# Kernel tuning notes

Measured on AMD Instinct MI355X. Metric: run time of the kernel, lower is better.

Reference implementation:

```python
import jax, jax.numpy as jnp
import numpy as np

B, S, D = 2, 2048, 1024   # batch, seq, d_model
E, F, K = 8, 2048, 2      # num_experts, ffn_hidden_size, top_k


def setup_inputs() -> dict:
    key = jax.random.key(0)
    ks = jax.random.split(key, 5)
    scale = 0.02
    hidden_states = jax.random.normal(ks[0], (B, S, D), dtype=jnp.float32)
    router_kernel = jax.random.normal(ks[1], (D, E), dtype=jnp.float32) * scale
    # expert params, already reshaped to (E, F, D) as in DbrxExpertGLU.expert_shape
    w1 = jax.random.normal(ks[2], (E, F, D), dtype=jnp.float32) * scale
    v1 = jax.random.normal(ks[3], (E, F, D), dtype=jnp.float32) * scale
    w2 = jax.random.normal(ks[4], (E, F, D), dtype=jnp.float32) * scale
    return {"hidden_states": hidden_states, "router_kernel": router_kernel,
            "w1": w1, "v1": v1, "w2": w2}


def reference(hidden_states, router_kernel, w1, v1, w2):
    # ---- Router ----
    logits = jnp.einsum('bsd,de->bse', hidden_states.astype(jnp.float32), router_kernel)
    weights = jax.nn.softmax(logits, axis=-1)                # [B,S,E]
    top_weights, top_experts = jax.lax.top_k(weights, K)     # [B,S,K]
    # moe_normalize_expert_weights = 1 -> L1 normalization
    top_weights = top_weights / jnp.sum(jnp.abs(top_weights), axis=-1, keepdims=True)
    weights = weights.astype(hidden_states.dtype)
    top_weights = top_weights.astype(hidden_states.dtype)
    # ---- Experts: every expert's GLU over all tokens, masked accumulation ----
    out = jnp.zeros_like(hidden_states)
    for e in range(E):  # small fixed expert count; matches original loop
        x1 = jnp.einsum('bsd,fd->bsf', hidden_states, w1[e])   # [B,S,F]
        x2 = jnp.einsum('bsd,fd->bsf', hidden_states, v1[e])
        h = jax.nn.silu(x1) * x2
        y_e = jnp.einsum('bsf,fd->bsd', h, w2[e])               # [B,S,D]
        gate = jnp.sum((top_experts == e) * top_weights, axis=-1)  # [B,S]
        out = out + gate[:, :, None] * y_e
    return out, weights
```

## Files before the change

### kernel.cpp

```cpp
#include <hip/hip_runtime.h>
#include <stdint.h>
#include <math.h>

#define NB 2
#define NS 2048
#define ND 1024
#define NE 8
#define NF 2048
#define NTOK (NB*NS)
#define EFD ((size_t)NE*NF*ND)
#define NROWS (2*NTOK)

typedef short bf16x8 __attribute__((ext_vector_type(8)));
typedef float f32x4 __attribute__((ext_vector_type(4)));

__device__ __forceinline__ unsigned short f2bf(float f) {
  unsigned u = __float_as_uint(f);
  unsigned r = (u + 0x7FFFu + ((u >> 16) & 1u)) >> 16;
  return (unsigned short)r;
}
__device__ __forceinline__ float bf2f(unsigned short s) {
  return __uint_as_float(((unsigned)s) << 16);
}

__device__ __forceinline__ void async16(unsigned short* lds, const unsigned short* g) {
  __builtin_amdgcn_global_load_lds(
      (const __attribute__((address_space(1))) unsigned int*)g,
      (__attribute__((address_space(3))) unsigned int*)lds, 16, 0, 0);
}

#define VMCNT(n) asm volatile("s_waitcnt vmcnt(" #n ")" ::: "memory")
#define LGKM0    asm volatile("s_waitcnt lgkmcnt(0)" ::: "memory")
#define SBAR     __builtin_amdgcn_s_barrier()
#define SCHED0   __builtin_amdgcn_sched_barrier(0)

__global__ void cvt_bf16(const float* __restrict__ src,
                         unsigned short* __restrict__ dst, int n4) {
  int i = blockIdx.x * blockDim.x + threadIdx.x;
  int stride = gridDim.x * blockDim.x;
  for (; i < n4; i += stride) {
    float4 v = ((const float4*)src)[i];
    ushort4 o;
    o.x = f2bf(v.x); o.y = f2bf(v.y); o.z = f2bf(v.z); o.w = f2bf(v.w);
    ((ushort4*)dst)[i] = o;
  }
}

__global__ void transpose_w2(const float* __restrict__ w2,
                             unsigned short* __restrict__ w2t) {
  __shared__ float tile[32][33];
  int e = blockIdx.z;
  int d0 = blockIdx.x * 32, f0 = blockIdx.y * 32;
  int tx = threadIdx.x, ty = threadIdx.y;
  const float* src = w2 + (size_t)e * NF * ND;
  unsigned short* dst = w2t + (size_t)e * ND * NF;
#pragma unroll
  for (int i = ty; i < 32; i += 8)
    tile[i][tx] = src[(size_t)(f0 + i) * ND + d0 + tx];
  __syncthreads();
#pragma unroll
  for (int i = ty; i < 32; i += 8)
    dst[(size_t)(d0 + i) * NF + f0 + tx] = f2bf(tile[tx][i]);
}

__global__ void router_kernel(const float* __restrict__ hs,
                              const float* __restrict__ rk,
                              float* __restrict__ wout,
                              float* __restrict__ tw,
                              int* __restrict__ choice,
                              unsigned short* __restrict__ hsb) {
  int lane = threadIdx.x;
  int tt = lane & 15, part = lane >> 4;
  int t = blockIdx.x * 16 + tt;
  const float4* hrow = (const float4*)(hs + (size_t)t * ND) + part * 64;
  ushort4* hb4 = (ushort4*)(hsb + (size_t)t * ND) + part * 64;
  const float4* rk4 = (const float4*)rk + part * 512;
  float acc[NE];
#pragma unroll
  for (int e = 0; e < NE; ++e) acc[e] = 0.f;
#pragma unroll 4
  for (int i = 0; i < 64; ++i) {
    float4 x = hrow[i];
    ushort4 o;
    o.x = f2bf(x.x); o.y = f2bf(x.y); o.z = f2bf(x.z); o.w = f2bf(x.w);
    hb4[i] = o;
    float xs[4] = {x.x, x.y, x.z, x.w};
#pragma unroll
    for (int j = 0; j < 4; ++j) {
      float4 r0 = rk4[i * 8 + j * 2];
      float4 r1 = rk4[i * 8 + j * 2 + 1];
      acc[0] += xs[j] * r0.x; acc[1] += xs[j] * r0.y;
      acc[2] += xs[j] * r0.z; acc[3] += xs[j] * r0.w;
      acc[4] += xs[j] * r1.x; acc[5] += xs[j] * r1.y;
      acc[6] += xs[j] * r1.z; acc[7] += xs[j] * r1.w;
    }
  }
#pragma unroll
  for (int e = 0; e < NE; ++e) {
    acc[e] += __shfl_xor(acc[e], 16, 64);
    acc[e] += __shfl_xor(acc[e], 32, 64);
  }
  if (part == 0) {
    float mx = acc[0]; int i0 = 0;
#pragma unroll
    for (int e = 1; e < NE; ++e) if (acc[e] > mx) { mx = acc[e]; i0 = e; }
    float m2 = -3.4e38f; int i1 = 0;
#pragma unroll
    for (int e = 0; e < NE; ++e) if (e != i0 && acc[e] > m2) { m2 = acc[e]; i1 = e; }
    float p[NE]; float den = 0.f;
#pragma unroll
    for (int e = 0; e < NE; ++e) { p[e] = expf(acc[e] - mx); den += p[e]; }
    float inv = 1.f / den;
#pragma unroll
    for (int e = 0; e < NE; ++e) { p[e] *= inv; wout[t * NE + e] = p[e]; }
    float w0 = p[i0], w1 = p[i1];
    float s = 1.f / (w0 + w1);
    tw[t * 2 + 0] = w0 * s;
    tw[t * 2 + 1] = w1 * s;
    choice[t] = i0 | (i1 << 4);
  }
}

__global__ void build_lists(const int* __restrict__ choice,
                            int* __restrict__ counts,
                            int* __restrict__ off,
                            int* __restrict__ list,
                            int* __restrict__ posn) {
  __shared__ int lcnt[NE];
  int tid = threadIdx.x;
  if (tid < NE) lcnt[tid] = 0;
  __syncthreads();
  int4 c4 = ((const int4*)choice)[tid];
  int cs[4] = {c4.x, c4.y, c4.z, c4.w};
#pragma unroll
  for (int j = 0; j < 4; ++j) {
    int t = tid * 4 + j;
    int e0 = cs[j] & 15, e1 = (cs[j] >> 4) & 15;
    int p0 = atomicAdd(&lcnt[e0], 1);
    list[e0 * NTOK + p0] = t << 1;
    int p1 = atomicAdd(&lcnt[e1], 1);
    list[e1 * NTOK + p1] = (t << 1) | 1;
    posn[t] = p0 | (p1 << 16);
  }
  __syncthreads();
  if (tid == 0) {
    int s = 0;
#pragma unroll
    for (int e = 0; e < NE; ++e) { counts[e] = lcnt[e]; off[e] = s; s += lcnt[e]; }
    off[NE] = s;
  }
}

__global__ __launch_bounds__(256, 2) void gemm_fused(
    const int* __restrict__ counts, const int* __restrict__ off,
    const int* __restrict__ list,
    const unsigned short* __restrict__ A,
    const unsigned short* __restrict__ B1,
    const unsigned short* __restrict__ B2,
    unsigned short* __restrict__ H) {
  int bid = blockIdx.x;
  int e = bid >> 9;
  int rem = bid & 511;
  int mt = rem >> 4, nt = rem & 15;
  int cnt = counts[e];
  if (mt * 128 >= cnt) return;
  int off_e = off[e];

  __shared__ unsigned short lds[2][12288];

  int tid = threadIdx.x;
  int wid = tid >> 6, lane = tid & 63;
  int wr = wid >> 1, wc = wid & 1;
  int l15 = lane & 15, l4 = lane >> 4;
  const int* mylist = list + e * NTOK;

  int trow = tid >> 2;
  int co = ((tid & 3) ^ ((tid >> 3) & 3)) * 8;
  const unsigned short* aS0;
  const unsigned short* aS1;
  {
    int r0 = mt * 128 + trow;
    int r1 = r0 + 64;
    if (r0 >= cnt) r0 = cnt - 1;
    if (r1 >= cnt) r1 = cnt - 1;
    int e0 = mylist[r0], e1 = mylist[r1];
    aS0 = A + (size_t)(e0 >> 1) * ND + co;
    aS1 = A + (size_t)(e1 >> 1) * ND + co;
  }
  const unsigned short* b1S0 = B1 + (size_t)e * NF * ND + (size_t)(nt * 128 + trow) * ND + co;
  const unsigned short* b1S1 = b1S0 + (size_t)64 * ND;
  const unsigned short* b2S0 = B2 + (size_t)e * NF * ND + (size_t)(nt * 128 + trow) * ND + co;
  const unsigned short* b2S1 = b2S0 + (size_t)64 * ND;

  int rowA[4], rowB[4];
#pragma unroll
  for (int mi = 0; mi < 4; ++mi) {
    int r = wr * 64 + mi * 16 + l15;
    rowA[mi] = r * 64 + ((l4 ^ ((r >> 1) & 3)) << 4);
  }
#pragma unroll
  for (int ni = 0; ni < 4; ++ni) {
    int r = wc * 64 + ni * 16 + l15;
    rowB[ni] = r * 64 + ((l4 ^ ((r >> 1) & 3)) << 4);
  }

  f32x4 acc1[4][4], acc2[4][4];
#pragma unroll
  for (int mi = 0; mi < 4; ++mi)
#pragma unroll
    for (int ni = 0; ni < 4; ++ni) {
      f32x4 z = {0.f, 0.f, 0.f, 0.f};
      acc1[mi][ni] = z; acc2[mi][ni] = z;
    }

  auto STAGE = [&](int c, int kt) {
    int ko = kt * 32;
    unsigned short* base = &lds[c][0] + tid * 8;
    async16(base,         aS0 + ko);
    async16(base + 2048,  aS1 + ko);
    async16(base + 4096,  b1S0 + ko);
    async16(base + 6144,  b1S1 + ko);
    async16(base + 8192,  b2S0 + ko);
    async16(base + 10240, b2S1 + ko);
  };

  const int kT = ND / 32;
  STAGE(0, 0); STAGE(1, 1);

  for (int kt = 0; kt < kT; ++kt) {
    int cur = kt & 1;
    if (kt + 1 < kT) { VMCNT(6); }
    else             { VMCNT(0); }
    SCHED0;
    SBAR;

    const char* la = (const char*)&lds[cur][0];
    const char* lb1 = la + 8192;
    const char* lb2 = la + 16384;
    bf16x8 a[4], b1[4], b2[4];
#pragma unroll
    for (int mi = 0; mi < 4; ++mi)
      a[mi] = *(const bf16x8*)(la + rowA[mi]);
#pragma unroll
    for (int ni = 0; ni < 4; ++ni) {
      b1[ni] = *(const bf16x8*)(lb1 + rowB[ni]);
      b2[ni] = *(const bf16x8*)(lb2 + rowB[ni]);
    }
    LGKM0;
    SCHED0;
    SBAR;
    if (kt + 2 < kT) STAGE(cur, kt + 2);

    __builtin_amdgcn_s_setprio(1);
#pragma unroll
    for (int mi = 0; mi < 4; ++mi)
#pragma unroll
      for (int ni = 0; ni < 4; ++ni) {
        acc1[mi][ni] = __builtin_amdgcn_mfma_f32_16x16x32_bf16(
            a[mi], b1[ni], acc1[mi][ni], 0, 0, 0);
        acc2[mi][ni] = __builtin_amdgcn_mfma_f32_16x16x32_bf16(
            a[mi], b2[ni], acc2[mi][ni], 0, 0, 0);
      }
    __builtin_amdgcn_s_setprio(0);
  }

  int rowbase = mt * 128 + wr * 64;
  int colbase = nt * 128 + wc * 64;
#pragma unroll
  for (int mi = 0; mi < 4; ++mi) {
#pragma unroll
    for (int j = 0; j < 4; ++j) {
      int r = rowbase + mi * 16 + l4 * 4 + j;
      if (r >= cnt) continue;
      size_t row = (size_t)(off_e + r);
#pragma unroll
      for (int ni = 0; ni < 4; ++ni) {
        int c = colbase + ni * 16 + l15;
        float x1 = acc1[mi][ni][j];
        float x2 = acc2[mi][ni][j];
        float h = (x1 / (1.f + expf(-x1))) * x2;
        H[row * NF + c] = f2bf(h);
      }
    }
  }
}

__global__ __launch_bounds__(256, 2) void gemm_p3(
    const int* __restrict__ counts, const int* __restrict__ off,
    const unsigned short* __restrict__ Ah,
    const unsigned short* __restrict__ Bw,
    unsigned short* __restrict__ Y) {
  int bid = blockIdx.x;
  int e = bid >> 8;
  int rem = bid & 255;
  int mt = rem >> 3;
  int code = rem & 7;
  int nt = code >> 1, kh = code & 1;
  int cnt = counts[e];
  if (mt * 128 >= cnt) return;
  int off_e = off[e];

  __shared__ unsigned short lds[2][12288];

  int tid = threadIdx.x;
  int wid = tid >> 6, lane = tid & 63;
  int wr = wid >> 1, wc = wid & 1;
  int l15 = lane & 15, l4 = lane >> 4;

  int trow = tid >> 2;
  int co = ((tid & 3) ^ ((tid >> 3) & 3)) * 8;
  const unsigned short* aS[2];
#pragma unroll
  for (int g = 0; g < 2; ++g) {
    int r = mt * 128 + g * 64 + trow;
    if (r >= cnt) r = cnt - 1;
    aS[g] = Ah + (size_t)(off_e + r) * NF + kh * 1024 + co;
  }
  const unsigned short* bS[4];
#pragma unroll
  for (int g = 0; g < 4; ++g) {
    int d = nt * 256 + g * 64 + trow;
    bS[g] = Bw + (size_t)e * ND * NF + (size_t)d * NF + kh * 1024 + co;
  }

  int rowA[4], rowB[8];
#pragma unroll
  for (int mi = 0; mi < 4; ++mi) {
    int r = wr * 64 + mi * 16 + l15;
    rowA[mi] = r * 64 + ((l4 ^ ((r >> 1) & 3)) << 4);
  }
#pragma unroll
  for (int ni = 0; ni < 8; ++ni) {
    int r = wc * 128 + ni * 16 + l15;
    rowB[ni] = 8192 + r * 64 + ((l4 ^ ((r >> 1) & 3)) << 4);
  }

  f32x4 acc[4][8];
#pragma unroll
  for (int mi = 0; mi < 4; ++mi)
#pragma unroll
    for (int ni = 0; ni < 8; ++ni) {
      f32x4 z = {0.f, 0.f, 0.f, 0.f};
      acc[mi][ni] = z;
    }

  auto STAGE = [&](int c, int kt) {
    int ko = kt * 32;
    unsigned short* base = &lds[c][0] + tid * 8;
    async16(base,         aS[0] + ko);
    async16(base + 2048,  aS[1] + ko);
    async16(base + 4096,  bS[0] + ko);
    async16(base + 6144,  bS[1] + ko);
    async16(base + 8192,  bS[2] + ko);
    async16(base + 10240, bS[3] + ko);
  };

  const int kT = 32;
  STAGE(0, 0); STAGE(1, 1);

  for (int kt = 0; kt < kT; ++kt) {
    int cur = kt & 1;
    if (kt + 1 < kT) { VMCNT(6); }
    else             { VMCNT(0); }
    SCHED0;
    SBAR;

    const char* buf = (const char*)&lds[cur][0];
    bf16x8 a[4], b[8];
#pragma unroll
    for (int mi = 0; mi < 4; ++mi)
      a[mi] = *(const bf16x8*)(buf + rowA[mi]);
#pragma unroll
    for (int ni = 0; ni < 8; ++ni)
      b[ni] = *(const bf16x8*)(buf + rowB[ni]);
    LGKM0;
    SCHED0;
    SBAR;
    if (kt + 2 < kT) STAGE(cur, kt + 2);

    __builtin_amdgcn_s_setprio(1);
#pragma unroll
    for (int mi = 0; mi < 4; ++mi)
#pragma unroll
      for (int ni = 0; ni < 8; ++ni)
        acc[mi][ni] = __builtin_amdgcn_mfma_f32_16x16x32_bf16(
            a[mi], b[ni], acc[mi][ni], 0, 0, 0);
    __builtin_amdgcn_s_setprio(0);
  }

  unsigned short* Yp = Y + (size_t)kh * NROWS * ND;
#pragma unroll
  for (int mi = 0; mi < 4; ++mi)
#pragma unroll
    for (int j = 0; j < 4; ++j) {
      int r = mt * 128 + wr * 64 + mi * 16 + l4 * 4 + j;
      if (r >= cnt) continue;
      size_t row = (size_t)(off_e + r);
#pragma unroll
      for (int ni = 0; ni < 8; ++ni) {
        int d = nt * 256 + wc * 128 + ni * 16 + l15;
        Yp[row * ND + d] = f2bf(acc[mi][ni][j]);
      }
    }
}

__global__ void combine_kernel(const unsigned short* __restrict__ yc,
                               const float* __restrict__ tw,
                               const int* __restrict__ choice,
                               const int* __restrict__ posn,
                               const int* __restrict__ off,
                               float* __restrict__ out) {
  int t = blockIdx.x;
  int tid = threadIdx.x;
  int ch = choice[t];
  int pp = posn[t];
  int e0 = ch & 15, e1 = (ch >> 4) & 15;
  size_t r0 = (size_t)(off[e0] + (pp & 0xffff));
  size_t r1 = (size_t)(off[e1] + (pp >> 16));
  float w0 = tw[t * 2], w1 = tw[t * 2 + 1];
  const size_t P = (size_t)NROWS * ND;
  ushort4 a0 = ((const ushort4*)(yc + r0 * ND))[tid];
  ushort4 b0 = ((const ushort4*)(yc + P + r0 * ND))[tid];
  ushort4 a1 = ((const ushort4*)(yc + r1 * ND))[tid];
  ushort4 b1 = ((const ushort4*)(yc + P + r1 * ND))[tid];
  float4 o;
  o.x = w0 * (bf2f(a0.x) + bf2f(b0.x)) + w1 * (bf2f(a1.x) + bf2f(b1.x));
  o.y = w0 * (bf2f(a0.y) + bf2f(b0.y)) + w1 * (bf2f(a1.y) + bf2f(b1.y));
  o.z = w0 * (bf2f(a0.z) + bf2f(b0.z)) + w1 * (bf2f(a1.z) + bf2f(b1.z));
  o.w = w0 * (bf2f(a0.w) + bf2f(b0.w)) + w1 * (bf2f(a1.w) + bf2f(b1.w));
  ((float4*)(out + (size_t)t * ND))[tid] = o;
}


extern "C" void kernel_launch(void* const* d_in, const int* in_sizes, int n_in,
                              void* d_out, int out_size, void* d_ws, size_t ws_size,
                              hipStream_t stream) {
  const float* hs = (const float*)d_in[0];
  const float* rk = (const float*)d_in[1];
  const float* w1 = (const float*)d_in[2];
  const float* v1 = (const float*)d_in[3];
  const float* w2 = (const float*)d_in[4];
  float* out = (float*)d_out;
  float* wout = out + (size_t)NTOK * ND;

  char* ws = (char*)d_ws;
  int* counts = (int*)(ws + 0);
  int* off = (int*)(ws + 64);
  int* choice = (int*)(ws + 128);
  int* posn = (int*)(ws + 16512);
  float* tw = (float*)(ws + 32896);
  int* list = (int*)(ws + 65664);
  unsigned short* hsb = (unsigned short*)(ws + 196736);
  unsigned short* w1b = (unsigned short*)(ws + 8585344);
  unsigned short* v1b = (unsigned short*)(ws + 42139776);
  unsigned short* w2t = (unsigned short*)(ws + 75694208);
  unsigned short* hcomp = (unsigned short*)(ws + 109248640);
  unsigned short* ycomp = (unsigned short*)(ws + 142803072);

  router_kernel<<<256, 64, 0, stream>>>(hs, rk, wout, tw, choice, hsb);
  build_lists<<<1, 1024, 0, stream>>>(choice, counts, off, list, posn);

  cvt_bf16<<<4096, 256, 0, stream>>>(w1, w1b, (int)(EFD / 4));
  cvt_bf16<<<4096, 256, 0, stream>>>(v1, v1b, (int)(EFD / 4));
  transpose_w2<<<dim3(ND / 32, NF / 32, NE), dim3(32, 8), 0, stream>>>(w2, w2t);

  gemm_fused<<<4096, 256, 0, stream>>>(counts, off, list, hsb, w1b, v1b, hcomp);

  gemm_p3<<<2048, 256, 0, stream>>>(counts, off, hcomp, w2t, ycomp);

  combine_kernel<<<NTOK, 256, 0, stream>>>(ycomp, tw, choice, posn, off, out);
}
```

Measured before the change: 271.4 us.

## Unify expert GEMMs into 256x256-tile 8-wave kernel with phased LDS pipeline

Replaces the two 128-row GEMM kernels with one templated 512-thread kernel that uses 256x256 output tiles, a 64-wide K step split into two sub-steps, and a phase-interleaved schedule. Each phase issues its async loads before its MFMAs, overlapping copies with compute. In the fused W1/V1 pass the B tile stacks the W1 and V1 rows, and the GLU is applied by exchanging the V1 accumulators through LDS. The aim is more operand reuse per byte loaded and fewer blocks. The cost is about 132KB of LDS per block, more register pressure, and more wasted work on partially filled 256-row expert tiles.

```diff
diff --git a/kernel.cpp b/kernel.cpp
--- a/kernel.cpp
+++ b/kernel.cpp
@@ -151,257 +151,206 @@
   }
 }
 
-__global__ __launch_bounds__(256, 2) void gemm_fused(
+template <int FUSED>
+__global__ __launch_bounds__(512, 2) void gemm8(
     const int* __restrict__ counts, const int* __restrict__ off,
     const int* __restrict__ list,
     const unsigned short* __restrict__ A,
     const unsigned short* __restrict__ B1,
     const unsigned short* __restrict__ B2,
-    unsigned short* __restrict__ H) {
+    unsigned short* __restrict__ H,
+    unsigned short* __restrict__ Y) {
   int bid = blockIdx.x;
-  int e = bid >> 9;
-  int rem = bid & 511;
-  int mt = rem >> 4, nt = rem & 15;
+  int e, mt, nt, kh = 0;
+  if (FUSED) { e = bid >> 7; int r = bid & 127; mt = r >> 4; nt = r & 15; }
+  else       { e = bid >> 6; int r = bid & 63;  mt = r >> 3; int c = r & 7; nt = c >> 1; kh = c & 1; }
   int cnt = counts[e];
-  if (mt * 128 >= cnt) return;
+  if (mt * 256 >= cnt) return;
   int off_e = off[e];
 
-  __shared__ unsigned short lds[2][12288];
+  __shared__ char smem[135168];
 
   int tid = threadIdx.x;
   int wid = tid >> 6, lane = tid & 63;
-  int wr = wid >> 1, wc = wid & 1;
+  int wm = wid >> 2, wn = wid & 3;
   int l15 = lane & 15, l4 = lane >> 4;
   const int* mylist = list + e * NTOK;
 
-  int trow = tid >> 2;
-  int co = ((tid & 3) ^ ((tid >> 3) & 3)) * 8;
-  const unsigned short* aS0;
-  const unsigned short* aS1;
+  const unsigned short* aS0; const unsigned short* aS1;
+  const unsigned short* bS0; const unsigned short* bS1;
   {
-    int r0 = mt * 128 + trow;
-    int r1 = r0 + 64;
-    if (r0 >= cnt) r0 = cnt - 1;
-    if (r1 >= cnt) r1 = cnt - 1;
-    int e0 = mylist[r0], e1 = mylist[r1];
-    aS0 = A + (size_t)(e0 >> 1) * ND + co;
-    aS1 = A + (size_t)(e1 >> 1) * ND + co;
-  }
-  const unsigned short* b1S0 = B1 + (size_t)e * NF * ND + (size_t)(nt * 128 + trow) * ND + co;
-  const unsigned short* b1S1 = b1S0 + (size_t)64 * ND;
-  const unsigned short* b2S0 = B2 + (size_t)e * NF * ND + (size_t)(nt * 128 + trow) * ND + co;
-  const unsigned short* b2S1 = b2S0 + (size_t)64 * ND;
-
-  int rowA[4], rowB[4];
-#pragma unroll
-  for (int mi = 0; mi < 4; ++mi) {
-    int r = wr * 64 + mi * 16 + l15;
-    rowA[mi] = r * 64 + ((l4 ^ ((r >> 1) & 3)) << 4);
+#pragma unroll
+    for (int i = 0; i < 2; ++i) {
+      int slot = tid + i * 512;
+      int row = slot >> 2;
+      int co = ((slot & 3) ^ (row & 3)) * 8;
+      const unsigned short* ap;
+      const unsigned short* bp;
+      int r = mt * 256 + row;
+      if (r >= cnt) r = cnt - 1;
+      if (FUSED) {
+        int entry = mylist[r];
+        ap = A + (size_t)(entry >> 1) * ND + co;
+        bp = (row < 128)
+           ? B1 + (size_t)e * NF * ND + (size_t)(nt * 128 + row) * ND + co
+           : B2 + (size_t)e * NF * ND + (size_t)(nt * 128 + row - 128) * ND + co;
+      } else {
+        ap = A + (size_t)(off_e + r) * NF + kh * 1024 + co;
+        bp = B1 + (size_t)e * ND * NF + (size_t)(nt * 256 + row) * NF + kh * 1024 + co;
+      }
+      if (i == 0) { aS0 = ap; bS0 = bp; } else { aS1 = ap; bS1 = bp; }
+    }
+  }
+
+  int offA[8], offB[4];
+#pragma unroll
+  for (int mi = 0; mi < 8; ++mi) {
+    int row = wm * 128 + mi * 16 + l15;
+    offA[mi] = row * 64 + ((l4 ^ (row & 3)) << 4);
   }
 #pragma unroll
   for (int ni = 0; ni < 4; ++ni) {
-    int r = wc * 64 + ni * 16 + l15;
-    rowB[ni] = r * 64 + ((l4 ^ ((r >> 1) & 3)) << 4);
-  }
-
-  f32x4 acc1[4][4], acc2[4][4];
-#pragma unroll
-  for (int mi = 0; mi < 4; ++mi)
+    int row = wn * 64 + ni * 16 + l15;
+    offB[ni] = row * 64 + ((l4 ^ (row & 3)) << 4);
+  }
+
+  f32x4 acc[8][4];
+#pragma unroll
+  for (int mi = 0; mi < 8; ++mi)
 #pragma unroll
     for (int ni = 0; ni < 4; ++ni) {
       f32x4 z = {0.f, 0.f, 0.f, 0.f};
-      acc1[mi][ni] = z; acc2[mi][ni] = z;
-    }
-
-  auto STAGE = [&](int c, int kt) {
-    int ko = kt * 32;
-    unsigned short* base = &lds[c][0] + tid * 8;
-    async16(base,         aS0 + ko);
-    async16(base + 2048,  aS1 + ko);
-    async16(base + 4096,  b1S0 + ko);
-    async16(base + 6144,  b1S1 + ko);
-    async16(base + 8192,  b2S0 + ko);
-    async16(base + 10240, b2S1 + ko);
+      acc[mi][ni] = z;
+    }
+
+  auto STAGE_A = [&](int buf, int ks, int tile) {
+    if (tile < 16) {
+      int ko = tile * 64 + ks * 32;
+      unsigned short* base = (unsigned short*)(smem + buf * 65536 + ks * 16384) + tid * 8;
+      async16(base, aS0 + ko);
+      async16(base + 4096, aS1 + ko);
+    }
   };
-
-  const int kT = ND / 32;
-  STAGE(0, 0); STAGE(1, 1);
-
-  for (int kt = 0; kt < kT; ++kt) {
-    int cur = kt & 1;
-    if (kt + 1 < kT) { VMCNT(6); }
-    else             { VMCNT(0); }
-    SCHED0;
-    SBAR;
-
-    const char* la = (const char*)&lds[cur][0];
-    const char* lb1 = la + 8192;
-    const char* lb2 = la + 16384;
-    bf16x8 a[4], b1[4], b2[4];
-#pragma unroll
-    for (int mi = 0; mi < 4; ++mi)
-      a[mi] = *(const bf16x8*)(la + rowA[mi]);
-#pragma unroll
-    for (int ni = 0; ni < 4; ++ni) {
-      b1[ni] = *(const bf16x8*)(lb1 + rowB[ni]);
-      b2[ni] = *(const bf16x8*)(lb2 + rowB[ni]);
-    }
-    LGKM0;
-    SCHED0;
-    SBAR;
-    if (kt + 2 < kT) STAGE(cur, kt + 2);
-
-    __builtin_amdgcn_s_setprio(1);
-#pragma unroll
-    for (int mi = 0; mi < 4; ++mi)
-#pragma unroll
-      for (int ni = 0; ni < 4; ++ni) {
-        acc1[mi][ni] = __builtin_amdgcn_mfma_f32_16x16x32_bf16(
-            a[mi], b1[ni], acc1[mi][ni], 0, 0, 0);
-        acc2[mi][ni] = __builtin_amdgcn_mfma_f32_16x16x32_bf16(
-            a[mi], b2[ni], acc2[mi][ni], 0, 0, 0);
+  auto STAGE_B = [&](int buf, int ks, int tile) {
+    if (tile < 16) {
+      int ko = tile * 64 + ks * 32;
+      unsigned short* base = (unsigned short*)(smem + buf * 65536 + 32768 + ks * 16384) + tid * 8;
+      async16(base, bS0 + ko);
+      async16(base + 4096, bS1 + ko);
+    }
+  };
+
+  STAGE_A(0, 0, 0); STAGE_B(0, 0, 0);
+  STAGE_A(0, 1, 0); STAGE_B(0, 1, 0);
+  STAGE_A(1, 0, 1); STAGE_B(1, 0, 1);
+  VMCNT(8);
+  SCHED0;
+  SBAR;
+
+  bf16x8 bq0, bq1, bq2, bq3;
+
+#define PH(Q, BUF, MIB, KS, STG, VMT) \
+  { \
+    const char* ab = smem + (BUF) * 65536 + (KS) * 16384; \
+    const char* bb = ab + 32768; \
+    bf16x8 a0 = *(const bf16x8*)(ab + offA[(MIB) + 0]); \
+    bf16x8 a1 = *(const bf16x8*)(ab + offA[(MIB) + 1]); \
+    bf16x8 a2 = *(const bf16x8*)(ab + offA[(MIB) + 2]); \
+    bf16x8 a3 = *(const bf16x8*)(ab + offA[(MIB) + 3]); \
+    if ((Q) % 2 == 0) { \
+      bq0 = *(const bf16x8*)(bb + offB[0]); \
+      bq1 = *(const bf16x8*)(bb + offB[1]); \
+      bq2 = *(const bf16x8*)(bb + offB[2]); \
+      bq3 = *(const bf16x8*)(bb + offB[3]); \
+    } \
+    STG; \
+    SBAR; \
+    LGKM0; SCHED0; \
+    __builtin_amdgcn_s_setprio(1); \
+    acc[(MIB)+0][0] = __builtin_amdgcn_mfma_f32_16x16x32_bf16(a0, bq0, acc[(MIB)+0][0], 0, 0, 0); \
+    acc[(MIB)+0][1] = __builtin_amdgcn_mfma_f32_16x16x32_bf16(a0, bq1, acc[(MIB)+0][1], 0, 0, 0); \
+    acc[(MIB)+0][2] = __builtin_amdgcn_mfma_f32_16x16x32_bf16(a0, bq2, acc[(MIB)+0][2], 0, 0, 0); \
+    acc[(MIB)+0][3] = __builtin_amdgcn_mfma_f32_16x16x32_bf16(a0, bq3, acc[(MIB)+0][3], 0, 0, 0); \
+    acc[(MIB)+1][0] = __builtin_amdgcn_mfma_f32_16x16x32_bf16(a1, bq0, acc[(MIB)+1][0], 0, 0, 0); \
+    acc[(MIB)+1][1] = __builtin_amdgcn_mfma_f32_16x16x32_bf16(a1, bq1, acc[(MIB)+1][1], 0, 0, 0); \
+    acc[(MIB)+1][2] = __builtin_amdgcn_mfma_f32_16x16x32_bf16(a1, bq2, acc[(MIB)+1][2], 0, 0, 0); \
+    acc[(MIB)+1][3] = __builtin_amdgcn_mfma_f32_16x16x32_bf16(a1, bq3, acc[(MIB)+1][3], 0, 0, 0); \
+    acc[(MIB)+2][0] = __builtin_amdgcn_mfma_f32_16x16x32_bf16(a2, bq0, acc[(MIB)+2][0], 0, 0, 0); \
+    acc[(MIB)+2][1] = __builtin_amdgcn_mfma_f32_16x16x32_bf16(a2, bq1, acc[(MIB)+2][1], 0, 0, 0); \
+    acc[(MIB)+2][2] = __builtin_amdgcn_mfma_f32_16x16x32_bf16(a2, bq2, acc[(MIB)+2][2], 0, 0, 0); \
+    acc[(MIB)+2][3] = __builtin_amdgcn_mfma_f32_16x16x32_bf16(a2, bq3, acc[(MIB)+2][3], 0, 0, 0); \
+    acc[(MIB)+3][0] = __builtin_amdgcn_mfma_f32_16x16x32_bf16(a3, bq0, acc[(MIB)+3][0], 0, 0, 0); \
+    acc[(MIB)+3][1] = __builtin_amdgcn_mfma_f32_16x16x32_bf16(a3, bq1, acc[(MIB)+3][1], 0, 0, 0); \
+    acc[(MIB)+3][2] = __builtin_amdgcn_mfma_f32_16x16x32_bf16(a3, bq2, acc[(MIB)+3][2], 0, 0, 0); \
+    acc[(MIB)+3][3] = __builtin_amdgcn_mfma_f32_16x16x32_bf16(a3, bq3, acc[(MIB)+3][3], 0, 0, 0); \
+    __builtin_amdgcn_s_setprio(0); \
+    VMT; \
+    SBAR; \
+  }
+
+  for (int j = 0; j < 8; ++j) {
+    int t1 = 2 * j + 1, t2 = 2 * j + 2, t3 = 2 * j + 3;
+    bool last = (j == 7);
+    PH(0, 0, 0, 0, STAGE_A(1, 1, t1), {});
+    PH(1, 0, 4, 0, STAGE_B(1, 1, t1), { VMCNT(8); SCHED0; });
+    PH(2, 0, 0, 1, STAGE_A(0, 0, t2), {});
+    PH(3, 0, 4, 1, STAGE_B(0, 0, t2), { if (last) { VMCNT(4); } else { VMCNT(8); } SCHED0; });
+    PH(4, 1, 0, 0, STAGE_A(0, 1, t2), {});
+    PH(5, 1, 4, 0, STAGE_B(0, 1, t2), { if (last) { VMCNT(0); } else { VMCNT(8); } SCHED0; });
+    PH(6, 1, 0, 1, STAGE_A(1, 0, t3), {});
+    PH(7, 1, 4, 1, STAGE_B(1, 0, t3), { if (!last) { VMCNT(8); SCHED0; } });
+  }
+#undef PH
+
+  if (FUSED) {
+    float* xl = (float*)smem;
+    if (wn >= 2) {
+#pragma unroll
+      for (int mi = 0; mi < 8; ++mi)
+#pragma unroll
+        for (int jj = 0; jj < 4; ++jj) {
+          int row = wm * 128 + mi * 16 + l4 * 4 + jj;
+#pragma unroll
+          for (int ni = 0; ni < 4; ++ni)
+            xl[row * 132 + (wn - 2) * 64 + ni * 16 + l15] = acc[mi][ni][jj];
+        }
+    }
+    __syncthreads();
+    if (wn < 2) {
+#pragma unroll
+      for (int mi = 0; mi < 8; ++mi)
+#pragma unroll
+        for (int jj = 0; jj < 4; ++jj) {
+          int row = wm * 128 + mi * 16 + l4 * 4 + jj;
+          int r = mt * 256 + row;
+          if (r >= cnt) continue;
+          size_t hrow = (size_t)(off_e + r);
+#pragma unroll
+          for (int ni = 0; ni < 4; ++ni) {
+            int col = wn * 64 + ni * 16 + l15;
+            float x1 = acc[mi][ni][jj];
+            float x2 = xl[row * 132 + col];
+            float h = (x1 / (1.f + expf(-x1))) * x2;
+            H[hrow * NF + nt * 128 + col] = f2bf(h);
+          }
+        }
+    }
+  } else {
+    unsigned short* Yp = Y + (size_t)kh * NROWS * ND;
+#pragma unroll
+    for (int mi = 0; mi < 8; ++mi)
+#pragma unroll
+      for (int jj = 0; jj < 4; ++jj) {
+        int r = mt * 256 + wm * 128 + mi * 16 + l4 * 4 + jj;
+        if (r >= cnt) continue;
+        size_t row = (size_t)(off_e + r);
+#pragma unroll
+        for (int ni = 0; ni < 4; ++ni) {
+          int d = nt * 256 + wn * 64 + ni * 16 + l15;
+          Yp[row * ND + d] = f2bf(acc[mi][ni][jj]);
+        }
       }
-    __builtin_amdgcn_s_setprio(0);
-  }
-
-  int rowbase = mt * 128 + wr * 64;
-  int colbase = nt * 128 + wc * 64;
-#pragma unroll
-  for (int mi = 0; mi < 4; ++mi) {
-#pragma unroll
-    for (int j = 0; j < 4; ++j) {
-      int r = rowbase + mi * 16 + l4 * 4 + j;
-      if (r >= cnt) continue;
-      size_t row = (size_t)(off_e + r);
-#pragma unroll
-      for (int ni = 0; ni < 4; ++ni) {
-        int c = colbase + ni * 16 + l15;
-        float x1 = acc1[mi][ni][j];
-        float x2 = acc2[mi][ni][j];
-        float h = (x1 / (1.f + expf(-x1))) * x2;
-        H[row * NF + c] = f2bf(h);
-      }
-    }
-  }
-}
-
-__global__ __launch_bounds__(256, 2) void gemm_p3(
-    const int* __restrict__ counts, const int* __restrict__ off,
-    const unsigned short* __restrict__ Ah,
-    const unsigned short* __restrict__ Bw,
-    unsigned short* __restrict__ Y) {
-  int bid = blockIdx.x;
-  int e = bid >> 8;
-  int rem = bid & 255;
-  int mt = rem >> 3;
-  int code = rem & 7;
-  int nt = code >> 1, kh = code & 1;
-  int cnt = counts[e];
-  if (mt * 128 >= cnt) return;
-  int off_e = off[e];
-
-  __shared__ unsigned short lds[2][12288];
-
-  int tid = threadIdx.x;
-  int wid = tid >> 6, lane = tid & 63;
-  int wr = wid >> 1, wc = wid & 1;
-  int l15 = lane & 15, l4 = lane >> 4;
-
-  int trow = tid >> 2;
-  int co = ((tid & 3) ^ ((tid >> 3) & 3)) * 8;
-  const unsigned short* aS[2];
-#pragma unroll
-  for (int g = 0; g < 2; ++g) {
-    int r = mt * 128 + g * 64 + trow;
-    if (r >= cnt) r = cnt - 1;
-    aS[g] = Ah + (size_t)(off_e + r) * NF + kh * 1024 + co;
-  }
-  const unsigned short* bS[4];
-#pragma unroll
-  for (int g = 0; g < 4; ++g) {
-    int d = nt * 256 + g * 64 + trow;
-    bS[g] = Bw + (size_t)e * ND * NF + (size_t)d * NF + kh * 1024 + co;
-  }
-
-  int rowA[4], rowB[8];
-#pragma unroll
-  for (int mi = 0; mi < 4; ++mi) {
-    int r = wr * 64 + mi * 16 + l15;
-    rowA[mi] = r * 64 + ((l4 ^ ((r >> 1) & 3)) << 4);
-  }
-#pragma unroll
-  for (int ni = 0; ni < 8; ++ni) {
-    int r = wc * 128 + ni * 16 + l15;
-    rowB[ni] = 8192 + r * 64 + ((l4 ^ ((r >> 1) & 3)) << 4);
-  }
-
-  f32x4 acc[4][8];
-#pragma unroll
-  for (int mi = 0; mi < 4; ++mi)
-#pragma unroll
-    for (int ni = 0; ni < 8; ++ni) {
-      f32x4 z = {0.f, 0.f, 0.f, 0.f};
-      acc[mi][ni] = z;
-    }
-
-  auto STAGE = [&](int c, int kt) {
-    int ko = kt * 32;
-    unsigned short* base = &lds[c][0] + tid * 8;
-    async16(base,         aS[0] + ko);
-    async16(base + 2048,  aS[1] + ko);
-    async16(base + 4096,  bS[0] + ko);
-    async16(base + 6144,  bS[1] + ko);
-    async16(base + 8192,  bS[2] + ko);
-    async16(base + 10240, bS[3] + ko);
-  };
-
-  const int kT = 32;
-  STAGE(0, 0); STAGE(1, 1);
-
-  for (int kt = 0; kt < kT; ++kt) {
-    int cur = kt & 1;
-    if (kt + 1 < kT) { VMCNT(6); }
-    else             { VMCNT(0); }
-    SCHED0;
-    SBAR;
-
-    const char* buf = (const char*)&lds[cur][0];
-    bf16x8 a[4], b[8];
-#pragma unroll
-    for (int mi = 0; mi < 4; ++mi)
-      a[mi] = *(const bf16x8*)(buf + rowA[mi]);
-#pragma unroll
-    for (int ni = 0; ni < 8; ++ni)
-      b[ni] = *(const bf16x8*)(buf + rowB[ni]);
-    LGKM0;
-    SCHED0;
-    SBAR;
-    if (kt + 2 < kT) STAGE(cur, kt + 2);
-
-    __builtin_amdgcn_s_setprio(1);
-#pragma unroll
-    for (int mi = 0; mi < 4; ++mi)
-#pragma unroll
-      for (int ni = 0; ni < 8; ++ni)
-        acc[mi][ni] = __builtin_amdgcn_mfma_f32_16x16x32_bf16(
-            a[mi], b[ni], acc[mi][ni], 0, 0, 0);
-    __builtin_amdgcn_s_setprio(0);
-  }
-
-  unsigned short* Yp = Y + (size_t)kh * NROWS * ND;
-#pragma unroll
-  for (int mi = 0; mi < 4; ++mi)
-#pragma unroll
-    for (int j = 0; j < 4; ++j) {
-      int r = mt * 128 + wr * 64 + mi * 16 + l4 * 4 + j;
-      if (r >= cnt) continue;
-      size_t row = (size_t)(off_e + r);
-#pragma unroll
-      for (int ni = 0; ni < 8; ++ni) {
-        int d = nt * 256 + wc * 128 + ni * 16 + l15;
-        Yp[row * ND + d] = f2bf(acc[mi][ni][j]);
-      }
-    }
+  }
 }
 
 __global__ void combine_kernel(const unsigned short* __restrict__ yc,
@@ -464,9 +413,11 @@
   cvt_bf16<<<4096, 256, 0, stream>>>(v1, v1b, (int)(EFD / 4));
   transpose_w2<<<dim3(ND / 32, NF / 32, NE), dim3(32, 8), 0, stream>>>(w2, w2t);
 
-  gemm_fused<<<4096, 256, 0, stream>>>(counts, off, list, hsb, w1b, v1b, hcomp);
-
-  gemm_p3<<<2048, 256, 0, stream>>>(counts, off, hcomp, w2t, ycomp);
+  gemm8<1><<<1024, 512, 0, stream>>>(counts, off, list, hsb, w1b, v1b,
+                                     hcomp, nullptr);
+
+  gemm8<0><<<512, 512, 0, stream>>>(counts, off, nullptr, hcomp, w2t, nullptr,
+                                    nullptr, ycomp);
 
   combine_kernel<<<NTOK, 256, 0, stream>>>(ycomp, tw, choice, posn, off, out);
 }
```

Result: slower. 306.5 us (+12.9%).
